# Kernel optimization log

Measured on AMD Instinct MI355X. Metric: run time of the kernel, lower is better.

The kernel has to match this reference:

```python
import jax, jax.numpy as jnp
import numpy as np

DIM = 4096
N_HEADS = 32
N_KV_HEADS = 8
HEAD_DIM = DIM // N_HEADS  # 128
B, S = 2, 2048
LN_EPS = 1e-5


def _precompute_freqs_cis(seqlen, head_dim, theta=10000.0):
    inv = 1.0 / (theta ** (np.arange(0, head_dim, 2, dtype=np.float32) / head_dim))  # [HD/2]
    ang = np.outer(np.arange(seqlen, dtype=np.float32), inv)  # [S, HD/2]
    return jnp.asarray(np.stack([np.cos(ang), np.sin(ang)], axis=-1))  # [S, HD/2, 2]


def setup_inputs() -> dict:
    key = jax.random.key(0)
    ks = jax.random.split(key, 9)
    std = 0.02
    return {
        "x": jax.random.normal(ks[0], (B, S, DIM), dtype=jnp.float32),
        "freqs_cis": _precompute_freqs_cis(S, HEAD_DIM),
        "wq": jax.random.normal(ks[1], (N_HEADS * HEAD_DIM, DIM), dtype=jnp.float32) * std,
        "wk": jax.random.normal(ks[2], (N_KV_HEADS * HEAD_DIM, DIM), dtype=jnp.float32) * std,
        "wv": jax.random.normal(ks[3], (N_KV_HEADS * HEAD_DIM, DIM), dtype=jnp.float32) * std,
        "wo": jax.random.normal(ks[4], (DIM, N_HEADS * HEAD_DIM), dtype=jnp.float32) * std,
        "q_norm_w": jnp.ones((N_HEADS * HEAD_DIM,), dtype=jnp.float32),
        "q_norm_b": jnp.zeros((N_HEADS * HEAD_DIM,), dtype=jnp.float32),
        "k_norm_w": jnp.ones((N_KV_HEADS * HEAD_DIM,), dtype=jnp.float32),
        "k_norm_b": jnp.zeros((N_KV_HEADS * HEAD_DIM,), dtype=jnp.float32),
    }


def _layernorm(v, w, b):
    mu = jnp.mean(v, axis=-1, keepdims=True)
    var = jnp.var(v, axis=-1, keepdims=True)
    return (v - mu) * jax.lax.rsqrt(var + LN_EPS) * w + b


def _rope(t, fc):
    # t: [B, S, nh, HD]; fc: [S, HD/2, 2] = (cos, sin)
    b_, s_, nh, hd = t.shape
    tr = t.reshape(b_, s_, nh, hd // 2, 2)
    a, bb = tr[..., 0], tr[..., 1]
    cos = fc[None, :, None, :, 0]
    sin = fc[None, :, None, :, 1]
    out = jnp.stack([a * cos - bb * sin, a * sin + bb * cos], axis=-1)
    return out.reshape(t.shape)


def reference(x, freqs_cis, wq, wk, wv, wo, q_norm_w, q_norm_b, k_norm_w, k_norm_b):
    bsz, seqlen, _ = x.shape
    H, KV, HD = N_HEADS, N_KV_HEADS, HEAD_DIM
    R = H // KV  # GQA repeat factor

    xq = jnp.einsum('bsd,ed->bse', x, wq)
    xk = jnp.einsum('bsd,ed->bse', x, wk)
    xv = jnp.einsum('bsd,ed->bse', x, wv)

    xq = _layernorm(xq, q_norm_w, q_norm_b)
    xk = _layernorm(xk, k_norm_w, k_norm_b)

    xq = xq.reshape(bsz, seqlen, H, HD)
    xk = xk.reshape(bsz, seqlen, KV, HD)
    xv = xv.reshape(bsz, seqlen, KV, HD)

    xq = _rope(xq, freqs_cis)
    xk = _rope(xk, freqs_cis)

    # GQA: group q heads as (kv, rep) and broadcast k/v instead of materializing repeats
    xqg = xq.reshape(bsz, seqlen, KV, R, HD)
    scale = 1.0 / jnp.sqrt(jnp.float32(HD))
    scores = jnp.einsum('bqkrh,bskh->bkrqs', xqg, xk) * scale  # [B,KV,R,S,S]
    attn = jax.nn.softmax(scores, axis=-1)
    out = jnp.einsum('bkrqs,bskh->bqkrh', attn, xv).reshape(bsz, seqlen, H * HD)
    return jnp.einsum('bse,de->bsd', out, wo)
```

## Files before the change

### kernel.cpp

```cpp
#include <hip/hip_runtime.h>
#include <cstdint>

typedef _Float16 half4v __attribute__((ext_vector_type(4)));
typedef _Float16 half8v __attribute__((ext_vector_type(8)));
typedef __fp16   fp16x2 __attribute__((ext_vector_type(2)));
typedef float    f32x4v __attribute__((ext_vector_type(4)));

#define DIM    4096
#define SEQ    2048
#define NBATCH 2
#define NHEAD  32
#define NKVH   8
#define HDIM   128
#define MROWS  (NBATCH*SEQ)
#define QKV_N  6144
#define KOFF   4096
#define VOFF   5120

__device__ __forceinline__ void gl_lds16(const _Float16* g, _Float16* l) {
  __builtin_amdgcn_global_load_lds(
      (const __attribute__((address_space(1))) void*)g,
      (__attribute__((address_space(3))) void*)l, 16, 0, 0);
}

__global__ __launch_bounds__(256) void cvt_kernel(const float* __restrict__ in,
                                                  _Float16* __restrict__ out, int n8) {
  int stride = gridDim.x * blockDim.x;
  for (int i = blockIdx.x * blockDim.x + threadIdx.x; i < n8; i += stride) {
    const float4* p = (const float4*)(in + (size_t)i * 8);
    float4 a = p[0], b = p[1];
    half8v h;
    h[0] = (_Float16)a.x; h[1] = (_Float16)a.y; h[2] = (_Float16)a.z; h[3] = (_Float16)a.w;
    h[4] = (_Float16)b.x; h[5] = (_Float16)b.y; h[6] = (_Float16)b.z; h[7] = (_Float16)b.w;
    *(half8v*)(out + (size_t)i * 8) = h;
  }
}


#define SBAR() do { asm volatile("" ::: "memory"); \
                    __builtin_amdgcn_s_barrier();  \
                    asm volatile("" ::: "memory"); } while (0)
#define LGK0() asm volatile("s_waitcnt lgkmcnt(0)" ::: "memory")
#define VM6()  asm volatile("s_waitcnt vmcnt(6)" ::: "memory")
#define VM0()  asm volatile("s_waitcnt vmcnt(0)" ::: "memory")

#define STAGE_HALF(Gm, rowbase, kidx, h, buf) do {                                   \
    gl_lds16((Gm) + (size_t)((rowbase) + (h)*128 + srow) * K + (kidx)*64 + sslot8,   \
             (buf) + (h)*8192 + w*512);                                              \
    gl_lds16((Gm) + (size_t)((rowbase) + (h)*128 + 64 + srow) * K + (kidx)*64 + sslot8, \
             (buf) + (h)*8192 + 4096 + w*512);                                       \
  } while (0)

#define MFMA_Q(hm, hn, bf)                                                   \
    _Pragma("unroll") for (int kk = 0; kk < 2; ++kk)                         \
      _Pragma("unroll") for (int mi = 0; mi < 4; ++mi)                       \
        _Pragma("unroll") for (int ni = 0; ni < 2; ++ni)                     \
          acc[(hm) * 4 + mi][(hn) * 2 + ni] =                                \
              __builtin_amdgcn_mfma_f32_16x16x32_f16(                        \
                  a[mi][kk], bf[ni][kk], acc[(hm) * 4 + mi][(hn) * 2 + ni], 0, 0, 0)

#define KSTEP(kcur, AC, BC, AN)                                              \
  do {                                                                       \
    const int k_ = (kcur);                                                   \
    half8v a[4][2], b0[2][2], b1[2][2];                                      \
                                         \
    _Pragma("unroll") for (int mi = 0; mi < 4; ++mi)                         \
      _Pragma("unroll") for (int kk = 0; kk < 2; ++kk)                       \
        a[mi][kk] = *(const half8v*)((AC) + (wm * 128 + mi * 16 + li) * 64 + \
                                     (((kk * 4 + g) ^ li7) * 8));            \
    _Pragma("unroll") for (int ni = 0; ni < 2; ++ni)                         \
      _Pragma("unroll") for (int kk = 0; kk < 2; ++kk)                       \
        b0[ni][kk] = *(const half8v*)((BC) + (wn * 64 + ni * 16 + li) * 64 + \
                                      (((kk * 4 + g) ^ li7) * 8));           \
    if (k_ + 1 < nkt) STAGE_HALF(A, bm, k_ + 1, 1, (AN));                    \
    SBAR(); LGK0();                                                          \
    __builtin_amdgcn_s_setprio(1);                                           \
    MFMA_Q(0, 0, b0);                                                        \
    __builtin_amdgcn_s_setprio(0);                                           \
    SBAR();                                                                  \
                                         \
    _Pragma("unroll") for (int ni = 0; ni < 2; ++ni)                         \
      _Pragma("unroll") for (int kk = 0; kk < 2; ++kk)                       \
        b1[ni][kk] = *(const half8v*)((BC) + (wn * 64 + 32 + ni * 16 + li) * 64 + \
                                      (((kk * 4 + g) ^ li7) * 8));           \
    SBAR(); LGK0();                                                          \
    __builtin_amdgcn_s_setprio(1);                                           \
    MFMA_Q(0, 1, b1);                                                        \
    __builtin_amdgcn_s_setprio(0);                                           \
    SBAR();                                                                  \
          \
    _Pragma("unroll") for (int mi = 0; mi < 4; ++mi)                         \
      _Pragma("unroll") for (int kk = 0; kk < 2; ++kk)                       \
        a[mi][kk] = *(const half8v*)((AC) + (wm * 128 + 64 + mi * 16 + li) * 64 + \
                                     (((kk * 4 + g) ^ li7) * 8));            \
    if (k_ + 2 < nkt) {                                                      \
      STAGE_HALF(B, bn, k_ + 2, 0, (BC));                                    \
      STAGE_HALF(B, bn, k_ + 2, 1, (BC));                                    \
    }                                                                        \
    SBAR(); LGK0();                                                          \
    __builtin_amdgcn_s_setprio(1);                                           \
    MFMA_Q(1, 1, b1);                                                        \
    __builtin_amdgcn_s_setprio(0);                                           \
    SBAR();                                                                  \
          \
    if (k_ + 2 < nkt) STAGE_HALF(A, bm, k_ + 2, 0, (AC));                    \
    SBAR();                                                                  \
    __builtin_amdgcn_s_setprio(1);                                           \
    MFMA_Q(1, 0, b0);                                                        \
    __builtin_amdgcn_s_setprio(0);                                           \
    if (k_ + 2 < nkt) { VM6(); } else if (k_ + 1 < nkt) { VM0(); }           \
    SBAR();                                                                  \
  } while (0)

template<int OUTF16>
__global__ __launch_bounds__(512, 2) void gemm256(const _Float16* __restrict__ A,
                                                  const _Float16* __restrict__ B,
                                                  void* __restrict__ Cp,
                                                  int N, int K, int nbx) {
  __shared__ __align__(16) _Float16 As[2][256 * 64];
  __shared__ __align__(16) _Float16 Bs[2][256 * 64];
  const int tid = threadIdx.x, lane = tid & 63, w = tid >> 6;
  const int g = lane >> 4, li = lane & 15, li7 = lane & 7;
  const int wm = w >> 2, wn = w & 3;
  const int nwg = gridDim.x, orig = blockIdx.x;
  const int wgid = (nwg & 7) ? orig : ((orig & 7) * (nwg >> 3) + (orig >> 3));
  const int bm = (wgid / nbx) * 256, bn = (wgid % nbx) * 256;
  const int srow = tid >> 3;
  const int sslot8 = ((lane & 7) ^ ((lane >> 3) & 7)) * 8;
  const int nkt = K >> 6;
  _Float16* As0 = &As[0][0]; _Float16* As1 = &As[1][0];
  _Float16* Bs0 = &Bs[0][0]; _Float16* Bs1 = &Bs[1][0];

  f32x4v acc[8][4] = {};

  STAGE_HALF(A, bm, 0, 0, As0);
  STAGE_HALF(A, bm, 0, 1, As0);
  STAGE_HALF(B, bn, 0, 0, Bs0);
  STAGE_HALF(B, bn, 0, 1, Bs0);
  if (nkt > 1) {
    STAGE_HALF(B, bn, 1, 0, Bs1);
    STAGE_HALF(B, bn, 1, 1, Bs1);
    STAGE_HALF(A, bm, 1, 0, As1);
    VM6();
  } else {
    VM0();
  }
  SBAR();

  for (int k = 0; k < nkt; k += 2) {
    KSTEP(k,     As0, Bs0, As1);
    KSTEP(k + 1, As1, Bs1, As0);
  }

  const int r0 = bm + wm * 128 + g * 4;
  const int c0 = bn + wn * 64 + li;
#pragma unroll
  for (int mi = 0; mi < 8; ++mi)
#pragma unroll
    for (int ni = 0; ni < 4; ++ni)
#pragma unroll
      for (int j = 0; j < 4; ++j) {
        size_t idx = (size_t)(r0 + mi * 16 + j) * N + (c0 + ni * 16);
        if (OUTF16) ((_Float16*)Cp)[idx] = (_Float16)acc[mi][ni][j];
        else        ((float*)Cp)[idx]    = acc[mi][ni][j];
      }
}

template<int E>
__global__ __launch_bounds__(256) void ln_rope(_Float16* __restrict__ t, int ldt,
                                               const float* __restrict__ gw,
                                               const float* __restrict__ gb,
                                               const float* __restrict__ fc) {
  constexpr int EPT = E / 256;
  const int row = blockIdx.x;
  const int s = row & (SEQ - 1);
  const int tid = threadIdx.x, lane = tid & 63, w = tid >> 6;
  _Float16* rp = t + (size_t)row * ldt + tid * EPT;
  float v[EPT];
#pragma unroll
  for (int i = 0; i < EPT; i += 4) {
    half4v hv = *(const half4v*)(rp + i);
    v[i] = (float)hv[0]; v[i+1] = (float)hv[1]; v[i+2] = (float)hv[2]; v[i+3] = (float)hv[3];
  }
  float sum = 0.f, ssq = 0.f;
#pragma unroll
  for (int i = 0; i < EPT; ++i) { sum += v[i]; ssq += v[i] * v[i]; }
#pragma unroll
  for (int off = 1; off < 64; off <<= 1) { sum += __shfl_xor(sum, off); ssq += __shfl_xor(ssq, off); }
  __shared__ float red[8];
  if (lane == 0) { red[w] = sum; red[4 + w] = ssq; }
  __syncthreads();
  sum = red[0] + red[1] + red[2] + red[3];
  ssq = red[4] + red[5] + red[6] + red[7];
  const float mu = sum * (1.0f / E);
  const float rstd = rsqrtf(ssq * (1.0f / E) - mu * mu + 1e-5f);
  float ov[EPT];
#pragma unroll
  for (int i = 0; i < EPT; i += 2) {
    int e = tid * EPT + i;
    int hd = e & (HDIM - 1);
    float2 cs = *(const float2*)(fc + (size_t)s * HDIM + (hd >> 1) * 2);
    float a = (v[i]   - mu) * rstd * gw[e]   + gb[e];
    float b = (v[i+1] - mu) * rstd * gw[e+1] + gb[e+1];
    ov[i]   = a * cs.x - b * cs.y;
    ov[i+1] = a * cs.y + b * cs.x;
  }
#pragma unroll
  for (int i = 0; i < EPT; i += 4) {
    half4v hv;
    hv[0] = (_Float16)ov[i];   hv[1] = (_Float16)ov[i+1];
    hv[2] = (_Float16)ov[i+2]; hv[3] = (_Float16)ov[i+3];
    *(half4v*)(rp + i) = hv;
  }
}

__global__ __launch_bounds__(256, 2) void attn_kernel(const _Float16* __restrict__ QKV,
                                                      _Float16* __restrict__ Oa) {
  __shared__ __align__(16) _Float16 Ksh[2][64 * 128];
  __shared__ __align__(16) char Vt[128 * 128];
  const int tid = threadIdx.x, lane = tid & 63, w = tid >> 6;
  const int g = lane >> 4, li = lane & 15;
  const int blk = blockIdx.x;
  const int qt = blk & 31, h = (blk >> 5) & 31, b = blk >> 10;
  const int kvh = h >> 2;
  const size_t LD = QKV_N;
  const _Float16* Qb = QKV + (size_t)(b * SEQ) * LD + h * HDIM;
  const _Float16* Kb = QKV + (size_t)(b * SEQ) * LD + KOFF + kvh * HDIM;
  const _Float16* Vb = QKV + (size_t)(b * SEQ) * LD + VOFF + kvh * HDIM;
  const int qrow = qt * 64 + w * 16 + li;
  half8v qf[4];
#pragma unroll
  for (int kk = 0; kk < 4; ++kk) {
    half8v q0 = *(const half8v*)(Qb + (size_t)qrow * LD + kk * 32 + g * 8);
#pragma unroll
    for (int e = 0; e < 8; ++e) q0[e] = q0[e] * (_Float16)0.08838834764831845f;
    qf[kk] = q0;
  }
  float mrow = -1e30f, lrow = 0.f;
  f32x4v oacc[8] = {};
  uint4 va[2], vb2[2];
  const int lg = lane >> 4;
  const int gbit = (lane >> 5) & 1;
#pragma unroll
  for (int i = 0; i < 4; ++i) {
    int chunk = i * 4 + w;
    int r = chunk * 4 + lg;
    int sc8 = ((lane & 15) ^ (r & 7)) * 8;
    gl_lds16(Kb + (size_t)r * LD + sc8, Ksh[0] + chunk * 512);
  }
#pragma unroll
  for (int i = 0; i < 2; ++i) {
    int p = tid + 256 * i; int v2 = p >> 4, c8 = p & 15;
    va[i]  = *(const uint4*)(Vb + (size_t)(v2 * 2)     * LD + c8 * 8);
    vb2[i] = *(const uint4*)(Vb + (size_t)(v2 * 2 + 1) * LD + c8 * 8);
  }
  const int NT = SEQ / 64;
  for (int kt = 0; kt < NT; ++kt) {
    __syncthreads();
#pragma unroll
    for (int i = 0; i < 2; ++i) {
      int p = tid + 256 * i; int v2 = p >> 4, c8 = p & 15;
      const uint32_t* a0 = (const uint32_t*)&va[i];
      const uint32_t* a1 = (const uint32_t*)&vb2[i];
      int slot = v2 >> 2, bofs = (v2 & 3) << 2;
#pragma unroll
      for (int wi = 0; wi < 4; ++wi) {
        uint32_t ev = __builtin_amdgcn_perm(a1[wi], a0[wi], 0x05040100u);
        uint32_t od = __builtin_amdgcn_perm(a1[wi], a0[wi], 0x07060302u);
        int hd0 = c8 * 8 + 2 * wi, hd1 = hd0 + 1;
        int k0 = ((hd0 >> 3) ^ hd0) & 7, k1 = ((hd1 >> 3) ^ hd1) & 7;
        *(uint32_t*)(Vt + hd0 * 128 + ((slot ^ k0) << 4) + bofs) = ev;
        *(uint32_t*)(Vt + hd1 * 128 + ((slot ^ k1) << 4) + bofs) = od;
      }
    }
    __syncthreads();
    if (kt + 1 < NT) {
#pragma unroll
      for (int i = 0; i < 2; ++i) {
        int p = tid + 256 * i; int v2 = p >> 4, c8 = p & 15;
        va[i]  = *(const uint4*)(Vb + (size_t)((kt + 1) * 64 + v2 * 2)     * LD + c8 * 8);
        vb2[i] = *(const uint4*)(Vb + (size_t)((kt + 1) * 64 + v2 * 2 + 1) * LD + c8 * 8);
      }
    }
    const _Float16* Kcur = Ksh[kt & 1];
    f32x4v sc[4] = {};
    __builtin_amdgcn_s_setprio(1);
#pragma unroll
    for (int kk = 0; kk < 4; ++kk) {
#pragma unroll
      for (int ni = 0; ni < 4; ++ni) {
        half8v kf = *(const half8v*)(Kcur + (16 * ni + li) * 128 + ((4 * kk + g) ^ (li & 7)) * 8);
        sc[ni] = __builtin_amdgcn_mfma_f32_16x16x32_f16(kf, qf[kk], sc[ni], 0, 0, 0);
      }
    }
    __builtin_amdgcn_s_setprio(0);
    if (kt + 1 < NT) {
      _Float16* Knxt = Ksh[(kt + 1) & 1];
#pragma unroll
      for (int i = 0; i < 4; ++i) {
        int chunk = i * 4 + w;
        int r = chunk * 4 + lg;
        int sc8 = ((lane & 15) ^ (r & 7)) * 8;
        gl_lds16(Kb + (size_t)((kt + 1) * 64 + r) * LD + sc8, Knxt + chunk * 512);
      }
    }
    float m16 = sc[0][0];
#pragma unroll
    for (int ni = 0; ni < 4; ++ni) {
      m16 = fmaxf(m16, fmaxf(fmaxf(sc[ni][0], sc[ni][1]), fmaxf(sc[ni][2], sc[ni][3])));
    }
    m16 = fmaxf(m16, __shfl_xor(m16, 16));
    m16 = fmaxf(m16, __shfl_xor(m16, 32));
    if (!__all(m16 - mrow <= 8.0f)) {
      const float mn = fmaxf(mrow, m16);
      const float sfo = __expf(mrow - mn);
      mrow = mn;
      lrow *= sfo;
      float sfj[4];
#pragma unroll
      for (int j = 0; j < 4; ++j) sfj[j] = __shfl(sfo, (lane & 48) | (4 * g + j));
#pragma unroll
      for (int nio = 0; nio < 8; ++nio) {
        oacc[nio][0] *= sfj[0]; oacc[nio][1] *= sfj[1];
        oacc[nio][2] *= sfj[2]; oacc[nio][3] *= sfj[3];
      }
    }
    float pp[4][4];
    float rs = 0.f;
#pragma unroll
    for (int ni = 0; ni < 4; ++ni)
#pragma unroll
      for (int j = 0; j < 4; ++j) { float pv = __expf(sc[ni][j] - mrow); pp[ni][j] = pv; rs += pv; }
    rs += __shfl_xor(rs, 16); rs += __shfl_xor(rs, 32);
    lrow += rs;
    uint32_t u[4][2];
#pragma unroll
    for (int ni = 0; ni < 4; ++ni) {
      fp16x2 p0 = __builtin_amdgcn_cvt_pkrtz(pp[ni][0], pp[ni][1]);
      fp16x2 p1 = __builtin_amdgcn_cvt_pkrtz(pp[ni][2], pp[ni][3]);
      u[ni][0] = *(uint32_t*)&p0;
      u[ni][1] = *(uint32_t*)&p1;
    }
#pragma unroll
    for (int kk = 0; kk < 2; ++kk) {
      uint32_t own0 = gbit ? u[2*kk+1][0] : u[2*kk][0];
      uint32_t own1 = gbit ? u[2*kk+1][1] : u[2*kk][1];
      uint32_t oth0 = gbit ? u[2*kk][0]   : u[2*kk+1][0];
      uint32_t oth1 = gbit ? u[2*kk][1]   : u[2*kk+1][1];
      uint32_t r16_0 = (uint32_t)__shfl_xor((int)own0, 16);
      uint32_t r16_1 = (uint32_t)__shfl_xor((int)own1, 16);
      uint32_t r32_0 = (uint32_t)__shfl_xor((int)oth0, 32);
      uint32_t r32_1 = (uint32_t)__shfl_xor((int)oth1, 32);
      uint32_t r48_0 = (uint32_t)__shfl_xor((int)oth0, 48);
      uint32_t r48_1 = (uint32_t)__shfl_xor((int)oth1, 48);
      uint32_t d0 = (g == 0) ? own0 : (g == 1) ? r48_0 : (g == 2) ? r32_0 : r16_0;
      uint32_t d1 = (g == 0) ? own1 : (g == 1) ? r48_1 : (g == 2) ? r32_1 : r16_1;
      uint32_t d2 = (g == 0) ? r16_0 : (g == 1) ? r32_0 : (g == 2) ? r48_0 : own0;
      uint32_t d3 = (g == 0) ? r16_1 : (g == 1) ? r32_1 : (g == 2) ? r48_1 : own1;
      union { uint32_t u4[4]; half8v h; } pa;
      pa.u4[0] = d0; pa.u4[1] = d1; pa.u4[2] = d2; pa.u4[3] = d3;
      __builtin_amdgcn_s_setprio(1);
#pragma unroll
      for (int nio = 0; nio < 8; ++nio) {
        int r = nio * 16 + li;
        int key = ((r >> 3) ^ r) & 7;
        half8v bv = *(const half8v*)(Vt + r * 128 + (((kk * 4 + g) ^ key) << 4));
        oacc[nio] = __builtin_amdgcn_mfma_f32_16x16x32_f16(pa.h, bv, oacc[nio], 0, 0, 0);
      }
      __builtin_amdgcn_s_setprio(0);
    }
  }
  float rinv[4];
#pragma unroll
  for (int j = 0; j < 4; ++j)
    rinv[j] = 1.0f / __shfl(lrow, (lane & 48) | (4 * g + j));
  _Float16* Ob = Oa + (size_t)(b * SEQ + qt * 64 + w * 16) * DIM + h * HDIM;
#pragma unroll
  for (int j = 0; j < 4; ++j)
#pragma unroll
    for (int nio = 0; nio < 8; ++nio)
      Ob[(size_t)(4 * g + j) * DIM + nio * 16 + li] = (_Float16)(oacc[nio][j] * rinv[j]);
}

extern "C" void kernel_launch(void* const* d_in, const int* in_sizes, int n_in,
                              void* d_out, int out_size, void* d_ws, size_t ws_size,
                              hipStream_t stream) {
  const float* x   = (const float*)d_in[0];
  const float* fc  = (const float*)d_in[1];
  const float* wq  = (const float*)d_in[2];
  const float* wk  = (const float*)d_in[3];
  const float* wv  = (const float*)d_in[4];
  const float* wo  = (const float*)d_in[5];
  const float* qnw = (const float*)d_in[6];
  const float* qnb = (const float*)d_in[7];
  const float* knw = (const float*)d_in[8];
  const float* knb = (const float*)d_in[9];
  float* out = (float*)d_out;
  (void)in_sizes; (void)n_in; (void)out_size;

  const size_t MB = 1024 * 1024;
  if (ws_size < 128 * MB) return;
  char* ws = (char*)d_ws;
  _Float16* x_h    = (_Float16*)(ws + 0);
  _Float16* wqkv_h = (_Float16*)(ws + 32 * MB);
  _Float16* wk_h   = (_Float16*)(ws + 64 * MB);
  _Float16* wv_h   = (_Float16*)(ws + 72 * MB);
  _Float16* qkv_h  = (_Float16*)(ws + 80 * MB);
  _Float16* wo_h   = wqkv_h;
  _Float16* ao_h   = x_h;

  cvt_kernel<<<2048, 256, 0, stream>>>(x,  x_h,    (MROWS * DIM) / 8);
  cvt_kernel<<<2048, 256, 0, stream>>>(wq, wqkv_h, (DIM * DIM) / 8);
  cvt_kernel<<<1024, 256, 0, stream>>>(wk, wk_h,   (1024 * DIM) / 8);
  cvt_kernel<<<1024, 256, 0, stream>>>(wv, wv_h,   (1024 * DIM) / 8);

  gemm256<1><<<(MROWS / 256) * (QKV_N / 256), 512, 0, stream>>>(x_h, wqkv_h, qkv_h,
                                                                QKV_N, DIM, QKV_N / 256);

  cvt_kernel<<<2048, 256, 0, stream>>>(wo, wo_h, (DIM * DIM) / 8);

  ln_rope<4096><<<MROWS, 256, 0, stream>>>(qkv_h,        QKV_N, qnw, qnb, fc);
  ln_rope<1024><<<MROWS, 256, 0, stream>>>(qkv_h + KOFF, QKV_N, knw, knb, fc);

  attn_kernel<<<NBATCH * NHEAD * (SEQ / 64), 256, 0, stream>>>(qkv_h, ao_h);

  gemm256<0><<<(MROWS / 256) * (DIM / 256), 512, 0, stream>>>(ao_h, wo_h, out,
                                                              DIM, DIM, DIM / 256);
}
```

Measured before the change: 689.0 us.

## Pre-transpose V in a separate kernel and async-load V tiles into double-buffered LDS

Adds a vtrans kernel that writes V once in head-dim-major layout into spare workspace. The attention kernel then loads V straight into a double-buffered LDS tile with global_load_lds, the same way it loads K. This replaces the per-tile register loads, byte permutes and LDS transpose stores, and cuts the loop to one barrier per iteration. In exchange it adds an extra kernel launch, one write and read of V in global memory, and doubles V's LDS footprint, which may lower occupancy.

```diff
diff --git a/kernel.cpp b/kernel.cpp
--- a/kernel.cpp
+++ b/kernel.cpp
@@ -17,7 +17,7 @@
 #define KOFF   4096
 #define VOFF   5120
 
-__device__ __forceinline__ void gl_lds16(const _Float16* g, _Float16* l) {
+__device__ __forceinline__ void gl_lds16(const void* g, void* l) {
   __builtin_amdgcn_global_load_lds(
       (const __attribute__((address_space(1))) void*)g,
       (__attribute__((address_space(3))) void*)l, 16, 0, 0);
@@ -214,10 +214,36 @@
   }
 }
 
+__global__ __launch_bounds__(256) void vtrans(const _Float16* __restrict__ qkv,
+                                              _Float16* __restrict__ vt) {
+  __shared__ _Float16 tile[64][136];
+  const int blk = blockIdx.x;
+  const int st = blk & 31, kvh = (blk >> 5) & 7, b = blk >> 8;
+  const int t = threadIdx.x;
+  const _Float16* src = qkv + (size_t)(b * SEQ + st * 64) * QKV_N + VOFF + kvh * 128;
+#pragma unroll
+  for (int i = 0; i < 4; ++i) {
+    int sl = (t >> 4) + i * 16;
+    int h0 = (t & 15) * 8;
+    *(half8v*)&tile[sl][h0] = *(const half8v*)(src + (size_t)sl * QKV_N + h0);
+  }
+  __syncthreads();
+  const int hd = t & 127, half = t >> 7;
+  _Float16* dst = vt + ((size_t)((b * NKVH + kvh) * 128 + hd)) * SEQ + st * 64 + half * 32;
+#pragma unroll
+  for (int j = 0; j < 32; j += 8) {
+    half8v v;
+#pragma unroll
+    for (int e = 0; e < 8; ++e) v[e] = tile[half * 32 + j + e][hd];
+    *(half8v*)(dst + j) = v;
+  }
+}
+
 __global__ __launch_bounds__(256, 2) void attn_kernel(const _Float16* __restrict__ QKV,
+                                                      const _Float16* __restrict__ VT,
                                                       _Float16* __restrict__ Oa) {
   __shared__ __align__(16) _Float16 Ksh[2][64 * 128];
-  __shared__ __align__(16) char Vt[128 * 128];
+  __shared__ __align__(16) char Vsh[2][128 * 128];
   const int tid = threadIdx.x, lane = tid & 63, w = tid >> 6;
   const int g = lane >> 4, li = lane & 15;
   const int blk = blockIdx.x;
@@ -226,7 +252,10 @@
   const size_t LD = QKV_N;
   const _Float16* Qb = QKV + (size_t)(b * SEQ) * LD + h * HDIM;
   const _Float16* Kb = QKV + (size_t)(b * SEQ) * LD + KOFF + kvh * HDIM;
-  const _Float16* Vb = QKV + (size_t)(b * SEQ) * LD + VOFF + kvh * HDIM;
+  const _Float16* VTb = VT + (size_t)((b * NKVH + kvh) * 128) * SEQ;
+  const int lg = lane >> 4;
+  const int gbit = (lane >> 5) & 1;
+
   const int qrow = qt * 64 + w * 16 + li;
   half8v qf[4];
 #pragma unroll
@@ -238,51 +267,38 @@
   }
   float mrow = -1e30f, lrow = 0.f;
   f32x4v oacc[8] = {};
-  uint4 va[2], vb2[2];
-  const int lg = lane >> 4;
-  const int gbit = (lane >> 5) & 1;
-#pragma unroll
-  for (int i = 0; i < 4; ++i) {
-    int chunk = i * 4 + w;
-    int r = chunk * 4 + lg;
-    int sc8 = ((lane & 15) ^ (r & 7)) * 8;
-    gl_lds16(Kb + (size_t)r * LD + sc8, Ksh[0] + chunk * 512);
-  }
-#pragma unroll
-  for (int i = 0; i < 2; ++i) {
-    int p = tid + 256 * i; int v2 = p >> 4, c8 = p & 15;
-    va[i]  = *(const uint4*)(Vb + (size_t)(v2 * 2)     * LD + c8 * 8);
-    vb2[i] = *(const uint4*)(Vb + (size_t)(v2 * 2 + 1) * LD + c8 * 8);
-  }
+
+#define ASTAGE_K(kt_, buf_) do {                                              \
+    _Pragma("unroll") for (int i_ = 0; i_ < 4; ++i_) {                        \
+      int chunk = i_ * 4 + w;                                                 \
+      int r = chunk * 4 + lg;                                                 \
+      int sc8 = ((lane & 15) ^ (r & 7)) * 8;                                  \
+      gl_lds16(Kb + (size_t)((kt_) * 64 + r) * LD + sc8, (buf_) + chunk * 512); \
+    } } while (0)
+
+#define ASTAGE_V(kt_, buf_) do {                                              \
+    _Pragma("unroll") for (int i_ = 0; i_ < 4; ++i_) {                        \
+      int chunk = i_ * 4 + w;                                                 \
+      int hd_ = chunk * 8 + (lane >> 3);                                      \
+      int keyh = (chunk ^ (lane >> 3)) & 7;                                   \
+      int p_ = lane & 7;                                                      \
+      gl_lds16(VTb + (size_t)hd_ * SEQ + (kt_) * 64 + ((p_ ^ keyh) * 8),      \
+               (buf_) + chunk * 1024);                                        \
+    } } while (0)
+
+  ASTAGE_K(0, Ksh[0]);
+  ASTAGE_V(0, Vsh[0]);
+  VM0();
+  SBAR();
+
   const int NT = SEQ / 64;
   for (int kt = 0; kt < NT; ++kt) {
-    __syncthreads();
-#pragma unroll
-    for (int i = 0; i < 2; ++i) {
-      int p = tid + 256 * i; int v2 = p >> 4, c8 = p & 15;
-      const uint32_t* a0 = (const uint32_t*)&va[i];
-      const uint32_t* a1 = (const uint32_t*)&vb2[i];
-      int slot = v2 >> 2, bofs = (v2 & 3) << 2;
-#pragma unroll
-      for (int wi = 0; wi < 4; ++wi) {
-        uint32_t ev = __builtin_amdgcn_perm(a1[wi], a0[wi], 0x05040100u);
-        uint32_t od = __builtin_amdgcn_perm(a1[wi], a0[wi], 0x07060302u);
-        int hd0 = c8 * 8 + 2 * wi, hd1 = hd0 + 1;
-        int k0 = ((hd0 >> 3) ^ hd0) & 7, k1 = ((hd1 >> 3) ^ hd1) & 7;
-        *(uint32_t*)(Vt + hd0 * 128 + ((slot ^ k0) << 4) + bofs) = ev;
-        *(uint32_t*)(Vt + hd1 * 128 + ((slot ^ k1) << 4) + bofs) = od;
-      }
-    }
-    __syncthreads();
+    const int cur = kt & 1;
     if (kt + 1 < NT) {
-#pragma unroll
-      for (int i = 0; i < 2; ++i) {
-        int p = tid + 256 * i; int v2 = p >> 4, c8 = p & 15;
-        va[i]  = *(const uint4*)(Vb + (size_t)((kt + 1) * 64 + v2 * 2)     * LD + c8 * 8);
-        vb2[i] = *(const uint4*)(Vb + (size_t)((kt + 1) * 64 + v2 * 2 + 1) * LD + c8 * 8);
-      }
-    }
-    const _Float16* Kcur = Ksh[kt & 1];
+      ASTAGE_K(kt + 1, Ksh[cur ^ 1]);
+      ASTAGE_V(kt + 1, Vsh[cur ^ 1]);
+    }
+    const _Float16* Kcur = Ksh[cur];
     f32x4v sc[4] = {};
     __builtin_amdgcn_s_setprio(1);
 #pragma unroll
@@ -294,16 +310,6 @@
       }
     }
     __builtin_amdgcn_s_setprio(0);
-    if (kt + 1 < NT) {
-      _Float16* Knxt = Ksh[(kt + 1) & 1];
-#pragma unroll
-      for (int i = 0; i < 4; ++i) {
-        int chunk = i * 4 + w;
-        int r = chunk * 4 + lg;
-        int sc8 = ((lane & 15) ^ (r & 7)) * 8;
-        gl_lds16(Kb + (size_t)((kt + 1) * 64 + r) * LD + sc8, Knxt + chunk * 512);
-      }
-    }
     float m16 = sc[0][0];
 #pragma unroll
     for (int ni = 0; ni < 4; ++ni) {
@@ -341,6 +347,7 @@
       u[ni][0] = *(uint32_t*)&p0;
       u[ni][1] = *(uint32_t*)&p1;
     }
+    const char* Vtcur = Vsh[cur];
 #pragma unroll
     for (int kk = 0; kk < 2; ++kk) {
       uint32_t own0 = gbit ? u[2*kk+1][0] : u[2*kk][0];
@@ -357,19 +364,23 @@
       uint32_t d1 = (g == 0) ? own1 : (g == 1) ? r48_1 : (g == 2) ? r32_1 : r16_1;
       uint32_t d2 = (g == 0) ? r16_0 : (g == 1) ? r32_0 : (g == 2) ? r48_0 : own0;
       uint32_t d3 = (g == 0) ? r16_1 : (g == 1) ? r32_1 : (g == 2) ? r48_1 : own1;
-      union { uint32_t u4[4]; half8v h; } pa;
+      union { uint32_t u4[4]; half8v hh; } pa;
       pa.u4[0] = d0; pa.u4[1] = d1; pa.u4[2] = d2; pa.u4[3] = d3;
       __builtin_amdgcn_s_setprio(1);
 #pragma unroll
       for (int nio = 0; nio < 8; ++nio) {
         int r = nio * 16 + li;
         int key = ((r >> 3) ^ r) & 7;
-        half8v bv = *(const half8v*)(Vt + r * 128 + (((kk * 4 + g) ^ key) << 4));
-        oacc[nio] = __builtin_amdgcn_mfma_f32_16x16x32_f16(pa.h, bv, oacc[nio], 0, 0, 0);
+        half8v bv = *(const half8v*)(Vtcur + r * 128 + (((kk * 4 + g) ^ key) << 4));
+        oacc[nio] = __builtin_amdgcn_mfma_f32_16x16x32_f16(pa.hh, bv, oacc[nio], 0, 0, 0);
       }
       __builtin_amdgcn_s_setprio(0);
     }
-  }
+    VM0();
+    SBAR();
+  }
+#undef ASTAGE_K
+#undef ASTAGE_V
   float rinv[4];
 #pragma unroll
   for (int j = 0; j < 4; ++j)
@@ -407,6 +418,7 @@
   _Float16* wv_h   = (_Float16*)(ws + 72 * MB);
   _Float16* qkv_h  = (_Float16*)(ws + 80 * MB);
   _Float16* wo_h   = wqkv_h;
+  _Float16* vt_h   = wk_h;
   _Float16* ao_h   = x_h;
 
   cvt_kernel<<<2048, 256, 0, stream>>>(x,  x_h,    (MROWS * DIM) / 8);
@@ -419,10 +431,12 @@
 
   cvt_kernel<<<2048, 256, 0, stream>>>(wo, wo_h, (DIM * DIM) / 8);
 
+  vtrans<<<NBATCH * NKVH * (SEQ / 64), 256, 0, stream>>>(qkv_h, vt_h);
+
   ln_rope<4096><<<MROWS, 256, 0, stream>>>(qkv_h,        QKV_N, qnw, qnb, fc);
   ln_rope<1024><<<MROWS, 256, 0, stream>>>(qkv_h + KOFF, QKV_N, knw, knb, fc);
 
-  attn_kernel<<<NBATCH * NHEAD * (SEQ / 64), 256, 0, stream>>>(qkv_h, ao_h);
+  attn_kernel<<<NBATCH * NHEAD * (SEQ / 64), 256, 0, stream>>>(qkv_h, vt_h, ao_h);
 
   gemm256<0><<<(MROWS / 256) * (DIM / 256), 512, 0, stream>>>(ao_h, wo_h, out,
                                                               DIM, DIM, DIM / 256);
```

Result: slower. 711.3 us (+3.2%).
